# Kernel tuning notes

Hardware: AMD Instinct MI355X
Metric: run time of the kernel (lower is better)

## Reference

```python
import jax, jax.numpy as jnp
import numpy as np

IN_DIM = 256
HID = 384
HEADS = 6
NH1 = HID // HEADS  # 64 per-head hidden in layer1
N = 3072
SLOPE_GAT = 0.2   # LeakyReLU inside GAT attention
SLOPE_ACT = 0.01  # default nn.LeakyReLU / F.leaky_relu slope


def _leaky(x, s):
    return jnp.where(x >= 0, x, s * x)


def _gat_sublayer(h, mask, W, a, heads, nh, concat):
    # h: [N, F_in], mask: [N, N] bool, W: [heads*nh, F_in], a: [2*nh]
    n = h.shape[0]
    g = (h @ W.T).reshape(n, heads, nh)  # [N, H, F]
    # e[i,j,h] = leakyrelu(<g_i, a_l> + <g_j, a_r>)  (avoids O(N^2) concat)
    sl = jnp.einsum('nhf,f->nh', g, a[:nh])
    sr = jnp.einsum('nhf,f->nh', g, a[nh:])
    e = _leaky(sl[:, None, :] + sr[None, :, :], SLOPE_GAT)  # [N, N, H]
    e = jnp.where(mask[:, :, None], e, jnp.float32(-10000.0))
    att = jax.nn.softmax(e, axis=1)  # softmax over source nodes j
    out = jnp.einsum('ijh,jhf->ihf', att, g)
    return out.reshape(n, heads * nh) if concat else out.mean(axis=1)


def _gat(x, mask, W1, a1, W2, a2):
    x = _gat_sublayer(x, mask, W1, a1, HEADS, NH1, True)   # [N, HID]
    x = jax.nn.elu(x)
    return _gat_sublayer(x, mask, W2, a2, 1, IN_DIM, False)  # [N, IN_DIM]


def setup_inputs() -> dict:
    key = jax.random.key(0)
    ks = iter(jax.random.split(key, 32))
    d = {
        'feature': jax.random.normal(next(ks), (1, N, IN_DIM), jnp.float32),
        'adj': jax.random.randint(next(ks), (1, N, N), 0, 2, jnp.int32),
        'doc_num': 16,
        'sect_num': 192,
    }
    def w(shape, scale=0.05):
        return jax.random.normal(next(ks), shape, jnp.float32) * scale
    for br in ('sent', 'sect', 'doc'):
        d[f'W1_{br}'] = w((HID, IN_DIM))
        d[f'a1_{br}'] = w((2 * NH1,))
        d[f'W2_{br}'] = w((IN_DIM, HID))
        d[f'a2_{br}'] = w((2 * IN_DIM,))
    d['fusion_W'] = w((IN_DIM, 3 * IN_DIM)); d['fusion_b'] = jnp.zeros((IN_DIM,), jnp.float32)
    d['ffn_W0'] = w((HID, IN_DIM)); d['ffn_b0'] = jnp.zeros((HID,), jnp.float32)
    d['ffn_W1'] = w((HID, HID)); d['ffn_b1'] = jnp.zeros((HID,), jnp.float32)
    d['ffn_W2'] = w((IN_DIM, HID)); d['ffn_b2'] = jnp.zeros((IN_DIM,), jnp.float32)
    return d


def reference(feature, adj, doc_num, sect_num,
              W1_sent, a1_sent, W2_sent, a2_sent,
              W1_sect, a1_sect, W2_sect, a2_sect,
              W1_doc, a1_doc, W2_doc, a2_doc,
              fusion_W, fusion_b,
              ffn_W0, ffn_b0, ffn_W1, ffn_b1, ffn_W2, ffn_b2):
    f = feature[0]          # [N, D]
    n = f.shape[0]
    A = adj[0] != 0         # [N, N]
    cols = jnp.arange(n)
    sent_mask = A & (cols < n - sect_num - doc_num)[None, :]
    sect_mask = A & (cols >= n - sect_num - doc_num)[None, :] & (cols < n - doc_num)[None, :]
    doc_mask = A & (cols >= n - doc_num)[None, :]

    f_sent = _gat(f, sent_mask, W1_sent, a1_sent, W2_sent, a2_sent) + f
    f_sect = _gat(f, sect_mask, W1_sect, a1_sect, W2_sect, a2_sect) + f
    f_doc = _gat(f, doc_mask, W1_doc, a1_doc, W2_doc, a2_doc) + f

    fused = jnp.concatenate([f_doc, f_sect, f_sent], axis=-1)  # [N, 3D]
    fused = _leaky(fused @ fusion_W.T + fusion_b, SLOPE_ACT)
    h = _leaky(fused @ ffn_W0.T + ffn_b0, SLOPE_ACT)
    h = _leaky(h @ ffn_W1.T + ffn_b1, SLOPE_ACT)
    h = _leaky(h @ ffn_W2.T + ffn_b2, SLOPE_ACT)
    return (h + f)[None]    # [1, N, D]
```

## Files before the change

### kernel.cpp

```cpp
#include <hip/hip_runtime.h>
#include <stdint.h>

#define N_NODES 3072
#define D_IN    256
#define HIDDEN  384
#define HEADS   6
#define NH1     64
#define C1      1152
#define C2      768
#define MASK_ULL   48
#define MASK_BYTES 384
#define MASK_BSTRIDE ((size_t)N_NODES * MASK_BYTES)
#define QS      6
#define LOG2E   1.4426950408889634f

typedef __bf16 bf16;
typedef __bf16 bf16x8 __attribute__((ext_vector_type(8)));
typedef __bf16 bf16x4 __attribute__((ext_vector_type(4)));
typedef float  f32x4  __attribute__((ext_vector_type(4)));

__device__ __forceinline__ void atomAddF(float* p, float v) {
  __hip_atomic_fetch_add(p, v, __ATOMIC_RELAXED, __HIP_MEMORY_SCOPE_AGENT);
}
__device__ __forceinline__ float fexp2(float x) {
  float r; asm("v_exp_f32 %0, %1" : "=v"(r) : "v"(x)); return r;
}
__device__ __forceinline__ int bnd32(int jlo, int jhi, int len, int q, int Qb) {
  return (q >= Qb) ? ((jhi + 31) & ~31) : ((jlo + (len * q) / Qb) & ~31);
}

struct CastArgs {
  const float* src[11];
  bf16*        dst[11];
  int          cum4[12];
};

__global__ __launch_bounds__(256) void cast_all_kernel(CastArgs A) {
  int g = blockIdx.x * 256 + threadIdx.x;
  int j = 0;
#pragma unroll
  for (int k = 1; k < 11; ++k) j += (g >= A.cum4[k]);
  int e = (g - A.cum4[j]) * 4;
  float4 v = *(const float4*)(A.src[j] + e);
  bf16x4 o = { (bf16)v.x, (bf16)v.y, (bf16)v.z, (bf16)v.w };
  *(bf16x4*)(A.dst[j] + e) = o;
}

__global__ __launch_bounds__(256) void pack_adj_kernel(const int* __restrict__ adj,
                                                       unsigned long long* __restrict__ maskU,
                                                       const int* __restrict__ dnum,
                                                       const int* __restrict__ snum) {
  int dn = dnum[0], sn = snum[0];
  int bb1 = N_NODES - sn - dn, bb2 = N_NODES - dn;
  int row = blockIdx.x;
  const int* ar = adj + (size_t)row * N_NODES;
  int lane = threadIdx.x & 63, wave = threadIdx.x >> 6;
#pragma unroll
  for (int it = 0; it < N_NODES / 256; ++it) {
    int j = it * 256 + wave * 64 + lane;
    bool a = ar[j] != 0;
    unsigned long long m0 = __ballot(a && (j < bb1));
    unsigned long long m1 = __ballot(a && (j >= bb1) && (j < bb2));
    unsigned long long m2 = __ballot(a && (j >= bb2));
    if (lane == 0) {
      size_t o = (size_t)row * MASK_ULL + it * 4 + wave;
      maskU[o] = m0;
      maskU[o + (size_t)N_NODES * MASK_ULL] = m1;
      maskU[o + 2 * (size_t)N_NODES * MASK_ULL] = m2;
    }
  }
}

template<int C>
__global__ __launch_bounds__(256) void pack_kernel(const bf16* __restrict__ src,
                                                   bf16* __restrict__ dst,
                                                   float* __restrict__ gm) {
  __shared__ bf16 t[64][72];
  int j0 = blockIdx.x * 64, f0 = blockIdx.y * 64;
  int rr = threadIdx.x >> 4;
  int cc = (threadIdx.x & 15) * 4;
#pragma unroll
  for (int p = 0; p < 4; ++p) {
    int r = p * 16 + rr;
    *(bf16x4*)&t[r][cc] = *(const bf16x4*)&src[(size_t)(j0 + r) * C + f0 + cc];
  }
  __syncthreads();
  int f = threadIdx.x & 63, g = threadIdx.x >> 6;
#pragma unroll
  for (int q = 0; q < 2; ++q) {
    int p = g * 2 + q;
    bf16x8 v = { t[p*8+0][f], t[p*8+1][f], t[p*8+2][f], t[p*8+3][f],
                 t[p*8+4][f], t[p*8+5][f], t[p*8+6][f], t[p*8+7][f] };
    *(bf16x8*)&dst[ ((size_t)((j0 >> 3) + p) * C + f0 + f) * 8 ] = v;
  }
  float s = 0.f;
#pragma unroll
  for (int k = 0; k < 16; ++k) s += (float)t[g * 16 + k][f];
  atomAddF(&gm[f0 + f], s * (1.0f / N_NODES));
}

template<int NCPB, int NH>
__global__ __launch_bounds__(256) void head_proj_kernel(
    const bf16* __restrict__ g, int ldg,
    const float* __restrict__ a0, const float* __restrict__ a1, const float* __restrict__ a2,
    float* __restrict__ elp, float* __restrict__ eln,
    float* __restrict__ erp, float* __restrict__ ern) {
  int c = blockIdx.y;
  int i = blockIdx.x * 16 + (threadIdx.x >> 4);
  int b = c / NCPB;
  const float* a = (b == 0) ? a0 : (b == 1) ? a1 : a2;
  int f0 = (threadIdx.x & 15) * (NH / 16);
  const bf16* gr = g + (size_t)i * ldg + c * NH + f0;
  float accl = 0.f, accr = 0.f;
#pragma unroll
  for (int k = 0; k < NH / 16; k += 4) {
    bf16x4 v = *(const bf16x4*)&gr[k];
#pragma unroll
    for (int e = 0; e < 4; ++e) {
      float gv = (float)v[e];
      accl += gv * a[f0 + k + e];
      accr += gv * a[NH + f0 + k + e];
    }
  }
#pragma unroll
  for (int m = 1; m < 16; m <<= 1) {
    accl += __shfl_xor(accl, m, 64);
    accr += __shfl_xor(accr, m, 64);
  }
  if ((threadIdx.x & 15) == 0) {
    int o = c * N_NODES + i;
    elp[o] = fexp2(accl * LOG2E);
    eln[o] = fexp2(0.2f * accl * LOG2E);
    erp[o] = fexp2(accr * LOG2E);
    ern[o] = fexp2(0.2f * accr * LOG2E);
  }
}

template<bool BIAS, bool LEAKY, bool RES, bool F32OUT>
__global__ __launch_bounds__(256) void gemm64_kernel(
    const bf16* __restrict__ A, int lda, int aZoff,
    const bf16* __restrict__ B0, const bf16* __restrict__ B1, const bf16* __restrict__ B2,
    int ldb, void* __restrict__ Cout, int ldc, int cZoff, int K,
    const float* __restrict__ bias, const float* __restrict__ res) {
  __shared__ bf16 As[64 * 64];
  __shared__ bf16 Bs[64 * 64];
  int z = blockIdx.z;
  const bf16* Ab = A + (size_t)z * aZoff;
  const bf16* Bb = (z == 0) ? B0 : (z == 1) ? B1 : B2;
  int m0 = blockIdx.x * 64, n0 = blockIdx.y * 64;
  int tid = threadIdx.x;
  int lane = tid & 63, wave = tid >> 6;
  int wm = wave >> 1, wn = wave & 1;
  int l15 = lane & 15, lk = lane >> 4;
  f32x4 acc[2][2] = {};
  for (int kt = 0; kt < K; kt += 64) {
#pragma unroll
    for (int h = 0; h < 2; ++h) {
      int u = h * 256 + tid;
      int r = u >> 3, up = u & 7;
      int ul = up ^ (r & 7);
      *(bf16x8*)&As[r * 64 + up * 8] = *(const bf16x8*)&Ab[(size_t)(m0 + r) * lda + kt + ul * 8];
      *(bf16x8*)&Bs[r * 64 + up * 8] = *(const bf16x8*)&Bb[(size_t)(n0 + r) * ldb + kt + ul * 8];
    }
    __syncthreads();
#pragma unroll
    for (int s = 0; s < 2; ++s) {
      bf16x8 af[2], bfr[2];
      int u = s * 4 + lk;
#pragma unroll
      for (int mi = 0; mi < 2; ++mi) {
        int r = wm * 32 + mi * 16 + l15;
        af[mi] = *(const bf16x8*)&As[r * 64 + (u ^ (r & 7)) * 8];
      }
#pragma unroll
      for (int ni = 0; ni < 2; ++ni) {
        int r = wn * 32 + ni * 16 + l15;
        bfr[ni] = *(const bf16x8*)&Bs[r * 64 + (u ^ (r & 7)) * 8];
      }
#pragma unroll
      for (int mi = 0; mi < 2; ++mi)
#pragma unroll
        for (int ni = 0; ni < 2; ++ni)
          acc[mi][ni] = __builtin_amdgcn_mfma_f32_16x16x32_bf16(af[mi], bfr[ni], acc[mi][ni], 0, 0, 0);
    }
    __syncthreads();
  }
#pragma unroll
  for (int mi = 0; mi < 2; ++mi)
#pragma unroll
    for (int ni = 0; ni < 2; ++ni)
#pragma unroll
      for (int r = 0; r < 4; ++r) {
        int i = m0 + wm * 32 + mi * 16 + lk * 4 + r;
        int col = z * cZoff + n0 + wn * 32 + ni * 16 + l15;
        float v = acc[mi][ni][r];
        if (BIAS) v += bias[col];
        if (LEAKY) v = (v >= 0.f) ? v : 0.01f * v;
        if (RES) v += res[(size_t)i * ldc + col];
        if (F32OUT) ((float*)Cout)[(size_t)i * ldc + col] = v;
        else        ((bf16*)Cout)[(size_t)i * ldc + col] = (bf16)v;
      }
}

struct Stream {
  float4 p0, p1, n0, n1;
  unsigned int m0, m1, m2, m3;
  bf16x8 b0, b1, b2, b3;
};

template<int C>
__device__ __forceinline__ void load_stream(
    Stream& s, int jb,
    const float* __restrict__ erpB, const float* __restrict__ ernB,
    const unsigned char* mr0, const unsigned char* mr1,
    const unsigned char* mr2, const unsigned char* mr3,
    const bf16* __restrict__ gPl) {
  s.p0 = *(const float4*)&erpB[jb];
  s.p1 = *(const float4*)&erpB[jb + 4];
  s.n0 = *(const float4*)&ernB[jb];
  s.n1 = *(const float4*)&ernB[jb + 4];
  int mo = jb >> 3;
  s.m0 = mr0[mo]; s.m1 = mr1[mo]; s.m2 = mr2[mo]; s.m3 = mr3[mo];
  const bf16* gp = gPl + (size_t)mo * C * 8;
  s.b0 = *(const bf16x8*)(gp + 0);
  s.b1 = *(const bf16x8*)(gp + 128);
  s.b2 = *(const bf16x8*)(gp + 256);
  s.b3 = *(const bf16x8*)(gp + 384);
}

template<bool L1>
__global__ __launch_bounds__(256) void att_kernel(
    const bf16* __restrict__ gP,
    const float* __restrict__ elpA, const float* __restrict__ elnA,
    const float* __restrict__ erpA, const float* __restrict__ ernA,
    const unsigned char* __restrict__ maskB,
    const int* __restrict__ dnum, const int* __restrict__ snum,
    float* __restrict__ accP, float* __restrict__ lP) {
  constexpr int C = L1 ? C1 : C2;
  int c = blockIdx.y;
  int b = L1 ? (c / 6) : (c >> 2);
  int colbase = L1 ? c * 64 : (b * 256 + (c & 3) * 64);
  int sidx = L1 ? c : b;
  int q = blockIdx.z;
  int Qb = (b == 0) ? QS : 1;
  if (q >= Qb) return;
  int dn = dnum[0], sn = snum[0];
  int bb1 = N_NODES - sn - dn, bb2 = N_NODES - dn;
  int jlo = (b == 0) ? 0 : (b == 1) ? bb1 : bb2;
  int jhi = (b == 0) ? bb1 : (b == 1) ? bb2 : N_NODES;
  int len = jhi - jlo;
  int wlo = bnd32(jlo, jhi, len, q, Qb);
  int whi = bnd32(jlo, jhi, len, q + 1, Qb);
  if (wlo >= whi) return;

  int wave = threadIdx.x >> 6, lane = threadIdx.x & 63;
  int l15 = lane & 15, lk = lane >> 4;
  int row0 = blockIdx.x * 256 + wave * 64;
  float elp[4], eln[4];
  const unsigned char* mr0;
  const unsigned char* mr1;
  const unsigned char* mr2;
  const unsigned char* mr3;
  {
    const unsigned char* mbase = maskB + (size_t)b * MASK_BSTRIDE;
#pragma unroll
    for (int rg = 0; rg < 4; ++rg) {
      int ip = row0 + rg * 16 + l15;
      elp[rg] = elpA[sidx * N_NODES + ip];
      eln[rg] = elnA[sidx * N_NODES + ip];
    }
    mr0 = mbase + (size_t)(row0 + 0 * 16 + l15) * MASK_BYTES;
    mr1 = mbase + (size_t)(row0 + 1 * 16 + l15) * MASK_BYTES;
    mr2 = mbase + (size_t)(row0 + 2 * 16 + l15) * MASK_BYTES;
    mr3 = mbase + (size_t)(row0 + 3 * 16 + l15) * MASK_BYTES;
  }
  const float* erpB = erpA + sidx * N_NODES;
  const float* ernB = ernA + sidx * N_NODES;
  const bf16* gPl = gP + (size_t)(colbase + l15) * 8;
  bf16x8 ones;
#pragma unroll
  for (int e = 0; e < 8; ++e) ones[e] = (bf16)1.0f;
  f32x4 acc[4][4] = {};
  f32x4 accl[4] = {};

  Stream s;
  load_stream<C>(s, wlo + lk * 8, erpB, ernB, mr0, mr1, mr2, mr3, gPl);
  for (int jt = wlo; jt < whi; jt += 32) {
    Stream cur = s;
    int nxt = jt + 32;
    if (nxt < whi) load_stream<C>(s, nxt + lk * 8, erpB, ernB, mr0, mr1, mr2, mr3, gPl);
    float pv[8] = { cur.p0.x, cur.p0.y, cur.p0.z, cur.p0.w, cur.p1.x, cur.p1.y, cur.p1.z, cur.p1.w };
    float nv[8] = { cur.n0.x, cur.n0.y, cur.n0.z, cur.n0.w, cur.n1.x, cur.n1.y, cur.n1.z, cur.n1.w };
#pragma unroll
    for (int rg = 0; rg < 4; ++rg) {
      unsigned int mb = (rg == 0) ? cur.m0 : (rg == 1) ? cur.m1 : (rg == 2) ? cur.m2 : cur.m3;
      bf16x8 a8;
#pragma unroll
      for (int e = 0; e < 8; ++e) {
        float z = elp[rg] * pv[e];
        float w = eln[rg] * nv[e];
        float p = (z >= 1.f) ? z : w;
        p = ((mb >> e) & 1u) ? p : 0.f;
        a8[e] = (bf16)p;
      }
      acc[rg][0] = __builtin_amdgcn_mfma_f32_16x16x32_bf16(a8, cur.b0, acc[rg][0], 0, 0, 0);
      acc[rg][1] = __builtin_amdgcn_mfma_f32_16x16x32_bf16(a8, cur.b1, acc[rg][1], 0, 0, 0);
      acc[rg][2] = __builtin_amdgcn_mfma_f32_16x16x32_bf16(a8, cur.b2, acc[rg][2], 0, 0, 0);
      acc[rg][3] = __builtin_amdgcn_mfma_f32_16x16x32_bf16(a8, cur.b3, acc[rg][3], 0, 0, 0);
      accl[rg] = __builtin_amdgcn_mfma_f32_16x16x32_bf16(a8, ones, accl[rg], 0, 0, 0);
    }
  }
  int slot = (b == 0) ? (c * QS + q) : (L1 ? (36 + (c - 6)) : (24 + (c - 4)));
  float* ap = accP + ((size_t)slot * N_NODES + row0) * 64;
#pragma unroll
  for (int rg = 0; rg < 4; ++rg)
#pragma unroll
    for (int nf = 0; nf < 4; ++nf)
#pragma unroll
      for (int r = 0; r < 4; ++r)
        ap[(rg * 16 + lk * 4 + r) * 64 + nf * 16 + l15] = acc[rg][nf][r];
  if (l15 == 0) {
#pragma unroll
    for (int rg = 0; rg < 4; ++rg)
#pragma unroll
      for (int r = 0; r < 4; ++r)
        lP[(size_t)slot * N_NODES + row0 + rg * 16 + lk * 4 + r] = accl[rg][r];
  }
}

__global__ __launch_bounds__(256) void fin1_kernel(
    const float* __restrict__ accP, const float* __restrict__ lP,
    const float* __restrict__ gm, const int* __restrict__ dnum, const int* __restrict__ snum,
    bf16* __restrict__ out1) {
  int t = blockIdx.x * 256 + threadIdx.x;
  int i = t / (C1 / 8), f0 = (t - i * (C1 / 8)) * 8;
  int c = f0 >> 6;
  int b = c / 6;
  int dn = dnum[0], sn = snum[0];
  int bb1 = N_NODES - sn - dn, bb2 = N_NODES - dn;
  int jlo = (b == 0) ? 0 : (b == 1) ? bb1 : bb2;
  int jhi = (b == 0) ? bb1 : (b == 1) ? bb2 : N_NODES;
  int len = jhi - jlo;
  int Qb = (b == 0) ? QS : 1;
  float l = 0.f;
  float a[8] = {0.f,0.f,0.f,0.f,0.f,0.f,0.f,0.f};
  if (len > 0) {
    for (int q = 0; q < Qb; ++q) {
      if (bnd32(jlo, jhi, len, q, Qb) >= bnd32(jlo, jhi, len, q + 1, Qb)) continue;
      int slot = (b == 0) ? (c * QS + q) : (36 + (c - 6));
      l += lP[(size_t)slot * N_NODES + i];
      const float* ap = &accP[((size_t)slot * N_NODES + i) * 64 + (f0 & 63)];
      f32x4 v0 = *(const f32x4*)ap, v1 = *(const f32x4*)(ap + 4);
#pragma unroll
      for (int e = 0; e < 4; ++e) { a[e] += v0[e]; a[e + 4] += v1[e]; }
    }
  }
  float inv = (l > 0.f) ? 1.f / l : 0.f;
  bf16x8 o;
#pragma unroll
  for (int e = 0; e < 8; ++e) {
    float v = (l > 0.f) ? a[e] * inv : gm[f0 + e];
    v = (v > 0.f) ? v : (__expf(v) - 1.f);
    o[e] = (bf16)v;
  }
  *(bf16x8*)&out1[(size_t)i * C1 + f0] = o;
}

__global__ __launch_bounds__(256) void fin2_kernel(
    const float* __restrict__ accP, const float* __restrict__ lP,
    const float* __restrict__ gm, const float* __restrict__ feat,
    const int* __restrict__ dnum, const int* __restrict__ snum,
    bf16* __restrict__ fused) {
  int t = blockIdx.x * 256 + threadIdx.x;
  int i = t / (C2 / 8), f0 = (t - i * (C2 / 8)) * 8;
  int b = f0 >> 8;
  int fi = f0 & 255;
  int fc = (f0 >> 6) & 3;
  int c = b * 4 + fc;
  int dn = dnum[0], sn = snum[0];
  int bb1 = N_NODES - sn - dn, bb2 = N_NODES - dn;
  int jlo = (b == 0) ? 0 : (b == 1) ? bb1 : bb2;
  int jhi = (b == 0) ? bb1 : (b == 1) ? bb2 : N_NODES;
  int len = jhi - jlo;
  int Qb = (b == 0) ? QS : 1;
  float l = 0.f;
  float a[8] = {0.f,0.f,0.f,0.f,0.f,0.f,0.f,0.f};
  if (len > 0) {
    for (int q = 0; q < Qb; ++q) {
      if (bnd32(jlo, jhi, len, q, Qb) >= bnd32(jlo, jhi, len, q + 1, Qb)) continue;
      int slot = (b == 0) ? (c * QS + q) : (24 + (c - 4));
      l += lP[(size_t)slot * N_NODES + i];
      const float* ap = &accP[((size_t)slot * N_NODES + i) * 64 + (f0 & 63)];
      f32x4 v0 = *(const f32x4*)ap, v1 = *(const f32x4*)(ap + 4);
#pragma unroll
      for (int e = 0; e < 4; ++e) { a[e] += v0[e]; a[e + 4] += v1[e]; }
    }
  }
  float inv = (l > 0.f) ? 1.f / l : 0.f;
  bf16x8 o;
#pragma unroll
  for (int e = 0; e < 8; ++e) {
    float v = (l > 0.f) ? a[e] * inv : gm[f0 + e];
    v += feat[(size_t)i * D_IN + fi + e];
    o[e] = (bf16)v;
  }
  *(bf16x8*)&fused[(size_t)i * C2 + (2 - b) * D_IN + fi] = o;
}

extern "C" void kernel_launch(void* const* d_in, const int* in_sizes, int n_in,
                              void* d_out, int out_size, void* d_ws, size_t ws_size,
                              hipStream_t stream) {
  (void)in_sizes; (void)n_in; (void)out_size; (void)ws_size;
  const float* feature = (const float*)d_in[0];
  const int*   adj     = (const int*)d_in[1];
  const int*   dnum    = (const int*)d_in[2];
  const int*   snum    = (const int*)d_in[3];
  const float* W1s = (const float*)d_in[4];  const float* a1s = (const float*)d_in[5];
  const float* W2s = (const float*)d_in[6];  const float* a2s = (const float*)d_in[7];
  const float* W1e = (const float*)d_in[8];  const float* a1e = (const float*)d_in[9];
  const float* W2e = (const float*)d_in[10]; const float* a2e = (const float*)d_in[11];
  const float* W1d = (const float*)d_in[12]; const float* a1d = (const float*)d_in[13];
  const float* W2d = (const float*)d_in[14]; const float* a2d = (const float*)d_in[15];
  const float* fW  = (const float*)d_in[16]; const float* fB  = (const float*)d_in[17];
  const float* w0  = (const float*)d_in[18]; const float* b0  = (const float*)d_in[19];
  const float* w1  = (const float*)d_in[20]; const float* b1  = (const float*)d_in[21];
  const float* w2  = (const float*)d_in[22]; const float* b2  = (const float*)d_in[23];

  char* ws = (char*)d_ws;
  size_t off = 0;
  auto alloc = [&](size_t bytes) { void* p = ws + off; off += (bytes + 255) & ~(size_t)255; return p; };

  unsigned long long* maskU = (unsigned long long*)alloc(3 * (size_t)N_NODES * MASK_ULL * 8);
  bf16* fbf   = (bf16*)alloc((size_t)N_NODES * D_IN * 2);
  bf16* w1b0  = (bf16*)alloc(HIDDEN * D_IN * 2);
  bf16* w1b1  = (bf16*)alloc(HIDDEN * D_IN * 2);
  bf16* w1b2  = (bf16*)alloc(HIDDEN * D_IN * 2);
  bf16* w2b0  = (bf16*)alloc(D_IN * HIDDEN * 2);
  bf16* w2b1  = (bf16*)alloc(D_IN * HIDDEN * 2);
  bf16* w2b2  = (bf16*)alloc(D_IN * HIDDEN * 2);
  bf16* wfusb = (bf16*)alloc(D_IN * C2 * 2);
  bf16* wf0b  = (bf16*)alloc(HIDDEN * D_IN * 2);
  bf16* wf1b  = (bf16*)alloc(HIDDEN * HIDDEN * 2);
  bf16* wf2b  = (bf16*)alloc(D_IN * HIDDEN * 2);
  bf16* g1    = (bf16*)alloc((size_t)N_NODES * C1 * 2);
  bf16* gP1   = (bf16*)alloc((size_t)N_NODES * C1 * 2);
  bf16* out1  = (bf16*)alloc((size_t)N_NODES * C1 * 2);
  bf16* g2    = (bf16*)alloc((size_t)N_NODES * C2 * 2);
  bf16* gP2   = (bf16*)alloc((size_t)N_NODES * C2 * 2);
  bf16* fusedB= (bf16*)alloc((size_t)N_NODES * C2 * 2);
  bf16* h0    = (bf16*)alloc((size_t)N_NODES * D_IN * 2);
  bf16* h1    = (bf16*)alloc((size_t)N_NODES * HIDDEN * 2);
  bf16* h2    = (bf16*)alloc((size_t)N_NODES * HIDDEN * 2);
  float* elp1 = (float*)alloc(18 * N_NODES * 4);
  float* eln1 = (float*)alloc(18 * N_NODES * 4);
  float* erp1 = (float*)alloc(18 * N_NODES * 4);
  float* ern1 = (float*)alloc(18 * N_NODES * 4);
  float* elp2 = (float*)alloc(3 * N_NODES * 4);
  float* eln2 = (float*)alloc(3 * N_NODES * 4);
  float* erp2 = (float*)alloc(3 * N_NODES * 4);
  float* ern2 = (float*)alloc(3 * N_NODES * 4);
  float* accU = (float*)alloc((size_t)48 * N_NODES * 64 * 4);
  float* lU   = (float*)alloc((size_t)48 * N_NODES * 4);
  size_t zoff = off;
  float* gm1  = (float*)alloc(C1 * 4);
  float* gm2  = (float*)alloc(C2 * 4);
  size_t zbytes = off - zoff;
  const unsigned char* maskBytes = (const unsigned char*)maskU;

  hipMemsetAsync(ws + zoff, 0, zbytes, stream);

  CastArgs ca;
  {
    const float* srcs[11] = { feature, W1s, W1e, W1d, W2s, W2e, W2d, fW, w0, w1, w2 };
    bf16* dsts[11] = { fbf, w1b0, w1b1, w1b2, w2b0, w2b1, w2b2, wfusb, wf0b, wf1b, wf2b };
    int counts[11] = { N_NODES*D_IN, HIDDEN*D_IN, HIDDEN*D_IN, HIDDEN*D_IN,
                       D_IN*HIDDEN, D_IN*HIDDEN, D_IN*HIDDEN, D_IN*C2,
                       HIDDEN*D_IN, HIDDEN*HIDDEN, D_IN*HIDDEN };
    int cum = 0;
    for (int k = 0; k < 11; ++k) { ca.src[k] = srcs[k]; ca.dst[k] = dsts[k]; ca.cum4[k] = cum; cum += counts[k] / 4; }
    ca.cum4[11] = cum;
    cast_all_kernel<<<cum / 256, 256, 0, stream>>>(ca);
  }
  pack_adj_kernel<<<N_NODES, 256, 0, stream>>>(adj, maskU, dnum, snum);
  gemm64_kernel<false,false,false,false><<<dim3(48,6,3), 256, 0, stream>>>(
      fbf, D_IN, 0, w1b0, w1b1, w1b2, D_IN, g1, C1, HIDDEN, D_IN, nullptr, nullptr);
  pack_kernel<C1><<<dim3(48,18), 256, 0, stream>>>(g1, gP1, gm1);
  head_proj_kernel<HEADS, NH1><<<dim3(192,18), 256, 0, stream>>>(g1, C1, a1s, a1e, a1d, elp1, eln1, erp1, ern1);
  att_kernel<true><<<dim3(12, 18, QS), 256, 0, stream>>>(gP1, elp1, eln1, erp1, ern1, maskBytes, dnum, snum, accU, lU);
  fin1_kernel<<<N_NODES * (C1 / 8) / 256, 256, 0, stream>>>(accU, lU, gm1, dnum, snum, out1);
  gemm64_kernel<false,false,false,false><<<dim3(48,4,3), 256, 0, stream>>>(
      out1, C1, HIDDEN, w2b0, w2b1, w2b2, HIDDEN, g2, C2, D_IN, HIDDEN, nullptr, nullptr);
  pack_kernel<C2><<<dim3(48,12), 256, 0, stream>>>(g2, gP2, gm2);
  head_proj_kernel<1, D_IN><<<dim3(192,3), 256, 0, stream>>>(g2, C2, a2s, a2e, a2d, elp2, eln2, erp2, ern2);
  att_kernel<false><<<dim3(12, 12, QS), 256, 0, stream>>>(gP2, elp2, eln2, erp2, ern2, maskBytes, dnum, snum, accU, lU);
  fin2_kernel<<<N_NODES * (C2 / 8) / 256, 256, 0, stream>>>(accU, lU, gm2, feature, dnum, snum, fusedB);
  gemm64_kernel<true,true,false,false><<<dim3(48,4,1), 256, 0, stream>>>(
      fusedB, C2, 0, wfusb, wfusb, wfusb, C2, h0, D_IN, 0, C2, fB, nullptr);
  gemm64_kernel<true,true,false,false><<<dim3(48,6,1), 256, 0, stream>>>(
      h0, D_IN, 0, wf0b, wf0b, wf0b, D_IN, h1, HIDDEN, 0, D_IN, b0, nullptr);
  gemm64_kernel<true,true,false,false><<<dim3(48,6,1), 256, 0, stream>>>(
      h1, HIDDEN, 0, wf1b, wf1b, wf1b, HIDDEN, h2, HIDDEN, 0, HIDDEN, b1, nullptr);
  gemm64_kernel<true,true,true,true><<<dim3(48,4,1), 256, 0, stream>>>(
      h2, HIDDEN, 0, wf2b, wf2b, wf2b, HIDDEN, d_out, D_IN, 0, HIDDEN, b2, feature);
}
```

Baseline: 285.5 us.

## Fuse cast and adjacency pack, double-buffer GEMM LDS, pipeline attention loads

Merges the weight/feature cast kernel and the adjacency bit-packing kernel into one launch, which saves a kernel launch and its gap. The GEMM now uses double-buffered shared-memory tiles: the next K tile is loaded into registers while MFMAs run on the current one, so only one barrier is needed per iteration. The attention kernel ping-pongs two register stream buffers instead of copying one, and gets a launch-bounds occupancy hint of 2 blocks per CU. The cost is doubled LDS in the GEMM and higher register pressure in the attention kernel, which may cause spills.

```diff
diff --git a/kernel.cpp b/kernel.cpp
--- a/kernel.cpp
+++ b/kernel.cpp
@@ -33,26 +33,28 @@
   const float* src[11];
   bf16*        dst[11];
   int          cum4[12];
+  int          castN;
 };
 
-__global__ __launch_bounds__(256) void cast_all_kernel(CastArgs A) {
-  int g = blockIdx.x * 256 + threadIdx.x;
-  int j = 0;
-#pragma unroll
-  for (int k = 1; k < 11; ++k) j += (g >= A.cum4[k]);
-  int e = (g - A.cum4[j]) * 4;
-  float4 v = *(const float4*)(A.src[j] + e);
-  bf16x4 o = { (bf16)v.x, (bf16)v.y, (bf16)v.z, (bf16)v.w };
-  *(bf16x4*)(A.dst[j] + e) = o;
-}
-
-__global__ __launch_bounds__(256) void pack_adj_kernel(const int* __restrict__ adj,
-                                                       unsigned long long* __restrict__ maskU,
-                                                       const int* __restrict__ dnum,
-                                                       const int* __restrict__ snum) {
+__global__ __launch_bounds__(256) void prep_kernel(CastArgs A,
+                                                   const int* __restrict__ adj,
+                                                   unsigned long long* __restrict__ maskU,
+                                                   const int* __restrict__ dnum,
+                                                   const int* __restrict__ snum) {
+  if ((int)blockIdx.x < A.castN) {
+    int g = blockIdx.x * 256 + threadIdx.x;
+    int j = 0;
+#pragma unroll
+    for (int k = 1; k < 11; ++k) j += (g >= A.cum4[k]);
+    int e = (g - A.cum4[j]) * 4;
+    float4 v = *(const float4*)(A.src[j] + e);
+    bf16x4 o = { (bf16)v.x, (bf16)v.y, (bf16)v.z, (bf16)v.w };
+    *(bf16x4*)(A.dst[j] + e) = o;
+    return;
+  }
   int dn = dnum[0], sn = snum[0];
   int bb1 = N_NODES - sn - dn, bb2 = N_NODES - dn;
-  int row = blockIdx.x;
+  int row = blockIdx.x - A.castN;
   const int* ar = adj + (size_t)row * N_NODES;
   int lane = threadIdx.x & 63, wave = threadIdx.x >> 6;
 #pragma unroll
@@ -142,8 +144,8 @@
     const bf16* __restrict__ B0, const bf16* __restrict__ B1, const bf16* __restrict__ B2,
     int ldb, void* __restrict__ Cout, int ldc, int cZoff, int K,
     const float* __restrict__ bias, const float* __restrict__ res) {
-  __shared__ bf16 As[64 * 64];
-  __shared__ bf16 Bs[64 * 64];
+  __shared__ bf16 As[2 * 64 * 64];
+  __shared__ bf16 Bs[2 * 64 * 64];
   int z = blockIdx.z;
   const bf16* Ab = A + (size_t)z * aZoff;
   const bf16* Bb = (z == 0) ? B0 : (z == 1) ? B1 : B2;
@@ -152,17 +154,35 @@
   int lane = tid & 63, wave = tid >> 6;
   int wm = wave >> 1, wn = wave & 1;
   int l15 = lane & 15, lk = lane >> 4;
+  int r0 = tid >> 3, p0 = tid & 7, q0 = p0 ^ (r0 & 7);
+  int r1 = (256 + tid) >> 3, p1 = tid & 7, q1 = p1 ^ (r1 & 7);
+  bf16x8 ra0, ra1, rb0, rb1;
+  auto gload = [&](int kt) {
+    const bf16* ab = Ab + (size_t)kt * 64;
+    const bf16* bb = Bb + (size_t)kt * 64;
+    ra0 = *(const bf16x8*)&ab[(size_t)(m0 + r0) * lda + q0 * 8];
+    ra1 = *(const bf16x8*)&ab[(size_t)(m0 + r1) * lda + q1 * 8];
+    rb0 = *(const bf16x8*)&bb[(size_t)(n0 + r0) * ldb + q0 * 8];
+    rb1 = *(const bf16x8*)&bb[(size_t)(n0 + r1) * ldb + q1 * 8];
+  };
+  auto sstore = [&](int buf) {
+    bf16* as = As + buf * 4096;
+    bf16* bs = Bs + buf * 4096;
+    *(bf16x8*)&as[r0 * 64 + p0 * 8] = ra0;
+    *(bf16x8*)&as[r1 * 64 + p1 * 8] = ra1;
+    *(bf16x8*)&bs[r0 * 64 + p0 * 8] = rb0;
+    *(bf16x8*)&bs[r1 * 64 + p1 * 8] = rb1;
+  };
   f32x4 acc[2][2] = {};
-  for (int kt = 0; kt < K; kt += 64) {
-#pragma unroll
-    for (int h = 0; h < 2; ++h) {
-      int u = h * 256 + tid;
-      int r = u >> 3, up = u & 7;
-      int ul = up ^ (r & 7);
-      *(bf16x8*)&As[r * 64 + up * 8] = *(const bf16x8*)&Ab[(size_t)(m0 + r) * lda + kt + ul * 8];
-      *(bf16x8*)&Bs[r * 64 + up * 8] = *(const bf16x8*)&Bb[(size_t)(n0 + r) * ldb + kt + ul * 8];
-    }
-    __syncthreads();
+  int nk = K >> 6;
+  gload(0);
+  sstore(0);
+  __syncthreads();
+  for (int kt = 0; kt < nk; ++kt) {
+    bool more = (kt + 1) < nk;
+    if (more) gload(kt + 1);
+    const bf16* as = As + (kt & 1) * 4096;
+    const bf16* bs = Bs + (kt & 1) * 4096;
 #pragma unroll
     for (int s = 0; s < 2; ++s) {
       bf16x8 af[2], bfr[2];
@@ -170,12 +190,12 @@
 #pragma unroll
       for (int mi = 0; mi < 2; ++mi) {
         int r = wm * 32 + mi * 16 + l15;
-        af[mi] = *(const bf16x8*)&As[r * 64 + (u ^ (r & 7)) * 8];
+        af[mi] = *(const bf16x8*)&as[r * 64 + (u ^ (r & 7)) * 8];
       }
 #pragma unroll
       for (int ni = 0; ni < 2; ++ni) {
         int r = wn * 32 + ni * 16 + l15;
-        bfr[ni] = *(const bf16x8*)&Bs[r * 64 + (u ^ (r & 7)) * 8];
+        bfr[ni] = *(const bf16x8*)&bs[r * 64 + (u ^ (r & 7)) * 8];
       }
 #pragma unroll
       for (int mi = 0; mi < 2; ++mi)
@@ -183,6 +203,7 @@
         for (int ni = 0; ni < 2; ++ni)
           acc[mi][ni] = __builtin_amdgcn_mfma_f32_16x16x32_bf16(af[mi], bfr[ni], acc[mi][ni], 0, 0, 0);
     }
+    if (more) sstore((kt + 1) & 1);
     __syncthreads();
   }
 #pragma unroll
@@ -229,7 +250,7 @@
 }
 
 template<bool L1>
-__global__ __launch_bounds__(256) void att_kernel(
+__global__ __launch_bounds__(256, 2) void att_kernel(
     const bf16* __restrict__ gP,
     const float* __restrict__ elpA, const float* __restrict__ elnA,
     const float* __restrict__ erpA, const float* __restrict__ ernA,
@@ -283,12 +304,7 @@
   f32x4 acc[4][4] = {};
   f32x4 accl[4] = {};
 
-  Stream s;
-  load_stream<C>(s, wlo + lk * 8, erpB, ernB, mr0, mr1, mr2, mr3, gPl);
-  for (int jt = wlo; jt < whi; jt += 32) {
-    Stream cur = s;
-    int nxt = jt + 32;
-    if (nxt < whi) load_stream<C>(s, nxt + lk * 8, erpB, ernB, mr0, mr1, mr2, mr3, gPl);
+  auto compute = [&](const Stream& cur) {
     float pv[8] = { cur.p0.x, cur.p0.y, cur.p0.z, cur.p0.w, cur.p1.x, cur.p1.y, cur.p1.z, cur.p1.w };
     float nv[8] = { cur.n0.x, cur.n0.y, cur.n0.z, cur.n0.w, cur.n1.x, cur.n1.y, cur.n1.z, cur.n1.w };
 #pragma unroll
@@ -309,7 +325,23 @@
       acc[rg][3] = __builtin_amdgcn_mfma_f32_16x16x32_bf16(a8, cur.b3, acc[rg][3], 0, 0, 0);
       accl[rg] = __builtin_amdgcn_mfma_f32_16x16x32_bf16(a8, ones, accl[rg], 0, 0, 0);
     }
-  }
+  };
+
+  Stream s0, s1;
+  load_stream<C>(s0, wlo + lk * 8, erpB, ernB, mr0, mr1, mr2, mr3, gPl);
+  int jt = wlo;
+  while (true) {
+    bool m1 = (jt + 32) < whi;
+    if (m1) load_stream<C>(s1, jt + 32 + lk * 8, erpB, ernB, mr0, mr1, mr2, mr3, gPl);
+    compute(s0);
+    if (!m1) break;
+    bool m2 = (jt + 64) < whi;
+    if (m2) load_stream<C>(s0, jt + 64 + lk * 8, erpB, ernB, mr0, mr1, mr2, mr3, gPl);
+    compute(s1);
+    if (!m2) break;
+    jt += 64;
+  }
+
   int slot = (b == 0) ? (c * QS + q) : (L1 ? (36 + (c - 6)) : (24 + (c - 4)));
   float* ap = accP + ((size_t)slot * N_NODES + row0) * 64;
 #pragma unroll
@@ -479,9 +511,9 @@
     int cum = 0;
     for (int k = 0; k < 11; ++k) { ca.src[k] = srcs[k]; ca.dst[k] = dsts[k]; ca.cum4[k] = cum; cum += counts[k] / 4; }
     ca.cum4[11] = cum;
-    cast_all_kernel<<<cum / 256, 256, 0, stream>>>(ca);
-  }
-  pack_adj_kernel<<<N_NODES, 256, 0, stream>>>(adj, maskU, dnum, snum);
+    ca.castN = cum / 256;
+    prep_kernel<<<ca.castN + N_NODES, 256, 0, stream>>>(ca, adj, maskU, dnum, snum);
+  }
   gemm64_kernel<false,false,false,false><<<dim3(48,6,3), 256, 0, stream>>>(
       fbf, D_IN, 0, w1b0, w1b1, w1b2, D_IN, g1, C1, HIDDEN, D_IN, nullptr, nullptr);
   pack_kernel<C1><<<dim3(48,18), 256, 0, stream>>>(g1, gP1, gm1);
```

After: 282.3 us. No clear change (-1.1%).
